# Kernel optimization log

Measured on AMD Instinct MI355X. Metric: run time of the kernel, lower is better.

Reference implementation:

```python
import jax, jax.numpy as jnp
import numpy as np


def setup_inputs() -> dict:
    key = jax.random.key(0)
    k0, k1, k2, k3 = jax.random.split(key, 4)
    N, D, DEG, B = 20000, 128, 32, 1024
    features = jax.random.normal(k0, (N, D), jnp.float32)
    neighbors = jax.random.randint(k1, (N, DEG), 0, N, dtype=jnp.int32)
    train_index = jax.random.randint(k2, (B,), 0, N, dtype=jnp.int32)
    W = jax.random.normal(k3, (1, 2 * D), jnp.float32) * (1.0 / np.sqrt(2 * D))
    b = jnp.zeros((1,), jnp.float32)
    return {"features": features, "W": W, "b": b, "neighbors": neighbors,
            "train_index": train_index, "walk_times": 8, "batch_size": B}


def reference(features, W, b, neighbors, train_index, walk_times, batch_size):
    N, D = features.shape
    B = train_index.shape[0]
    rows = jnp.arange(B)[:, None]                       # [B,1]
    self_oh = jax.nn.one_hot(train_index, N, dtype=jnp.float32)  # [B,N]

    # Dense adjacency rows of the start nodes (== adj_sparse[batch] densified)
    nb0 = neighbors[train_index]                        # [B,deg]
    adj0 = jnp.zeros((B, N), jnp.float32).at[rows, nb0].set(1.0)

    chosen = self_oh                                    # visited mask (start node marked)
    candi_mask = (adj0 - chosen) > 0.0                  # non-self candidates

    # Per-edge learned score: relu(Linear(concat(f_x, f_y))) == relu(fx@Wx + fy@Wy + b)
    Wx, Wy = W[0, :D], W[0, D:]
    sx = features[train_index] @ Wx                     # [B]
    sy = features[nb0] @ Wy                             # [B,deg]
    s = jax.nn.relu(sx[:, None] + sy + b[0])            # [B,deg]
    scored = jnp.zeros((B, N), jnp.float32).at[rows, nb0].set(s)
    candi = jnp.where(candi_mask, scored, 0.0)
    # rows with no (or all-zero-scored) candidates fall back to a self-loop of weight 1
    candi = jnp.where((candi.sum(axis=1) == 0.0)[:, None], self_oh, candi)

    keys = jax.random.split(jax.random.key(42), walk_times)

    def step(carry, k):
        candi, chosen = carry
        # degenerate rows: resample the start node (safe fallback for empty support)
        p = jnp.where((candi.sum(axis=1) == 0.0)[:, None], self_oh, candi)
        # multinomial(p, 1) via Gumbel-max (categorical with probs proportional to p)
        logp = jnp.where(p > 0.0, jnp.log(jnp.where(p > 0.0, p, 1.0)), -jnp.inf)
        g = jax.random.gumbel(k, (p.shape[0], p.shape[1]), jnp.float32)
        new = jnp.argmax(logp + g, axis=1)              # [B]
        chosen = jnp.maximum(chosen, jax.nn.one_hot(new, p.shape[1], dtype=jnp.float32))
        adj_new = jnp.zeros_like(candi).at[rows, neighbors[new]].set(1.0)
        candi = ((candi - chosen + adj_new) > 0.0).astype(jnp.float32)
        return (candi, chosen), new

    (_, _), steps = jax.lax.scan(step, (candi, chosen), keys)  # steps: [T,B]
    walks = jnp.concatenate(
        [train_index[:, None].astype(jnp.int32), steps.T.astype(jnp.int32)], axis=1)
    return walks
```

## Files before the change

kernel.cpp:

```cpp
#include <hip/hip_runtime.h>
#include <cstdint>

namespace {

constexpr int N    = 20000;
constexpr int D    = 128;
constexpr int DEG  = 32;
constexpr int BB   = 1024;
constexpr int T    = 8;
constexpr int NW   = (N + 31) / 32;
constexpr int MAXC = 384;

__device__ __forceinline__ uint32_t rotl32(uint32_t x, int n) {
  return (x << n) | (x >> (32 - n));
}

__device__ __forceinline__ void threefry2x32(uint32_t k0, uint32_t k1,
                                             uint32_t x0, uint32_t x1,
                                             uint32_t& o0, uint32_t& o1) {
  const uint32_t ks2 = k0 ^ k1 ^ 0x1BD11BDAu;
  x0 += k0; x1 += k1;
#define TF_ROUND(r) { x0 += x1; x1 = rotl32(x1, (r)); x1 ^= x0; }
  TF_ROUND(13) TF_ROUND(15) TF_ROUND(26) TF_ROUND(6)
  x0 += k1;  x1 += ks2 + 1u;
  TF_ROUND(17) TF_ROUND(29) TF_ROUND(16) TF_ROUND(24)
  x0 += ks2; x1 += k0 + 2u;
  TF_ROUND(13) TF_ROUND(15) TF_ROUND(26) TF_ROUND(6)
  x0 += k0;  x1 += k1 + 3u;
  TF_ROUND(17) TF_ROUND(29) TF_ROUND(16) TF_ROUND(24)
  x0 += k1;  x1 += ks2 + 4u;
  TF_ROUND(13) TF_ROUND(15) TF_ROUND(26) TF_ROUND(6)
  x0 += ks2; x1 += k0 + 5u;
#undef TF_ROUND
  o0 = x0; o1 = x1;
}

__device__ __forceinline__ uint32_t rbits(uint32_t k0, uint32_t k1, uint32_t j) {
  uint32_t o0, o1;
  threefry2x32(k0, k1, 0u, j, o0, o1);
  return o0 ^ o1;
}

__device__ __forceinline__ float gumbel_f32(uint32_t bits) {
  const uint32_t mant = bits >> 9;
  const float u = (mant == 0u) ? 1.17549435e-38f
                               : (__uint_as_float(0x3F800000u | mant) - 1.0f);
  const float inner = -(float)log((double)u);
  return -(float)log((double)inner);
}

__device__ __forceinline__ uint32_t f2ord(float f) {
  const uint32_t b = __float_as_uint(f);
  return (b & 0x80000000u) ? ~b : (b | 0x80000000u);
}

template <int CTRL>
__device__ __forceinline__ uint32_t dppmov(uint32_t v) {
  return (uint32_t)__builtin_amdgcn_update_dpp((int)v, (int)v, CTRL, 0xF, 0xF, false);
}

__device__ __forceinline__ void wave_max64(uint32_t& hi, uint32_t& lo) {
#define RL(CTRL) { const uint32_t oh = dppmov<CTRL>(hi), ol = dppmov<CTRL>(lo); \
    if (oh > hi || (oh == hi && ol > lo)) { hi = oh; lo = ol; } }
  RL(0x111) RL(0x112) RL(0x114) RL(0x118) RL(0x142) RL(0x143)
#undef RL
  hi = (uint32_t)__builtin_amdgcn_readlane((int)hi, 63);
  lo = (uint32_t)__builtin_amdgcn_readlane((int)lo, 63);
}

__global__ __launch_bounds__(64)
void walk_kernel(const float* __restrict__ features,
                 const float* __restrict__ W,
                 const float* __restrict__ bptr,
                 const int*   __restrict__ neighbors,
                 const int*   __restrict__ train_index,
                 int* __restrict__ out)
{
  __shared__ uint32_t candM[NW];
  __shared__ uint32_t chosenM[NW];
  __shared__ int      lst[2][MAXC];
  __shared__ float    val0[DEG];
  __shared__ int      pendC[16];
  __shared__ float    pendV[16];

  const int lane = threadIdx.x;
  const int r    = blockIdx.x;
  const int self = train_index[r];
  const uint32_t rN = (uint32_t)(r * N);
  const uint64_t lower = (1ULL << lane) - 1ULL;

  int nbj = -1;
  if (lane < DEG) nbj = neighbors[(size_t)self * DEG + lane];

  for (int i = lane; i < NW; i += 64) { candM[i] = 0u; chosenM[i] = 0u; }

  uint32_t sk0, sk1;
  threefry2x32(0u, 42u, 0u, (uint32_t)lane, sk0, sk1);

  const float bval = bptr[0];
  const float* frow = features + (size_t)self * D;
  float acc = frow[lane] * W[lane] + frow[lane + 64] * W[lane + 64];
  for (int m = 1; m < 64; m <<= 1) acc += __shfl_xor(acc, m);
  const float sx = acc;

  float sval = 0.0f;
  if (lane < DEG) {
    const float* g  = features + (size_t)nbj * D;
    const float* wy = W + D;
    float a = 0.0f;
    for (int d = 0; d < D; d += 4) {
      const float4 f = *reinterpret_cast<const float4*>(g + d);
      const float4 w = *reinterpret_cast<const float4*>(wy + d);
      a += f.x * w.x; a += f.y * w.y; a += f.z * w.z; a += f.w * w.w;
    }
    sval = fmaxf((sx + a) + bval, 0.0f);
  }

  bool add0 = false;
  if (lane < DEG && nbj != self && sval > 0.0f) {
    const uint32_t w = (uint32_t)nbj >> 5, bit = 1u << (nbj & 31);
    const uint32_t old = atomicOr(&candM[w], bit);
    add0 = !(old & bit);
  }
  const uint64_t m0 = __ballot(add0);
  if (add0) {
    const int p = (int)__popcll(m0 & lower);
    lst[0][p] = nbj; val0[p] = sval;
  }
  int cnt = (int)__popcll(m0);
  if (lane == 0) {
    chosenM[(uint32_t)self >> 5] |= 1u << (self & 31);
    if (cnt == 0) {
      lst[0][0] = self; val0[0] = 1.0f;
      candM[(uint32_t)self >> 5] |= 1u << (self & 31);
    }
  }
  if (cnt == 0) cnt = 1;

  int cur = 0;
  for (int k = 0; k < T; ++k) {
    const uint32_t kk0 = (uint32_t)__builtin_amdgcn_readlane((int)sk0, k);
    const uint32_t kk1 = (uint32_t)__builtin_amdgcn_readlane((int)sk1, k);

    uint32_t hi = 0u, lo = 0u;
    if (k == 0) {
      for (int i = lane; i < cnt; i += 64) {
        const int c = lst[cur][i];
        const float v = (float)log((double)val0[i])
                      + gumbel_f32(rbits(kk0, kk1, rN + (uint32_t)c));
        const uint32_t h = f2ord(v), l = 0x7FFFFFFFu - (uint32_t)c;
        if (h > hi || (h == hi && l > lo)) { hi = h; lo = l; }
      }
    } else {
      for (int i = lane; i < cnt; i += 128) {
        const int c = lst[cur][i];
        const uint32_t h = rbits(kk0, kk1, rN + (uint32_t)c) >> 9;
        const uint32_t l = 0x7FFFFFFFu - (uint32_t)c;
        uint32_t h2 = 0u, l2 = 0u;
        const int i2 = i + 64;
        if (i2 < cnt) {
          const int c2 = lst[cur][i2];
          h2 = rbits(kk0, kk1, rN + (uint32_t)c2) >> 9;
          l2 = 0x7FFFFFFFu - (uint32_t)c2;
        }
        if (h  > hi || (h  == hi && l  > lo)) { hi = h;  lo = l;  }
        if (h2 > hi || (h2 == hi && l2 > lo)) { hi = h2; lo = l2; }
      }
    }
    wave_max64(hi, lo);
    const int nn = (lo == 0u) ? self : (int)(0x7FFFFFFFu - lo);

    int nb = -1;
    if (lane < DEG) nb = neighbors[(size_t)nn * DEG + lane];

    if (lane == 0) {
      out[r * (T + 1) + k + 1] = nn;
      chosenM[(uint32_t)nn >> 5] |= 1u << (nn & 31);
    }

    int nc = 0, pc = 0;
    for (int i0 = 0; i0 < cnt; i0 += 64) {
      const int i = i0 + lane;
      const bool valid = (i < cnt);
      int c = 0;
      if (valid) c = lst[cur][i];
      bool keep = false, pnd = false;
      if (valid) {
        const uint32_t w = (uint32_t)c >> 5, bit = 1u << (c & 31);
        const bool ch = (c == nn) || ((chosenM[w] & bit) != 0u);
        keep = !ch; pnd = ch;
      }
      const uint64_t mk = __ballot(keep);
      const uint64_t mp = __ballot(pnd);
      if (keep) lst[cur ^ 1][nc + (int)__popcll(mk & lower)] = c;
      if (pnd) {
        const int q = pc + (int)__popcll(mp & lower);
        pendC[q] = c; pendV[q] = (k == 0) ? val0[i] : 1.0f;
      }
      nc += (int)__popcll(mk); pc += (int)__popcll(mp);
    }

    for (int q = 0; q < pc; ++q) {
      const int p = pendC[q];
      const float v = pendV[q];
      const bool isadj = __any(lane < DEG && nb == p);
      if ((v - 1.0f) + (isadj ? 1.0f : 0.0f) > 0.0f) {
        if (lane == 0) lst[cur ^ 1][nc] = p;
        ++nc;
      }
    }

    bool added = false;
    if (lane < DEG && nb != nn) {
      const uint32_t w = (uint32_t)nb >> 5, bit = 1u << (nb & 31);
      if (!(chosenM[w] & bit) && !(candM[w] & bit)) {
        const uint32_t old = atomicOr(&candM[w], bit);
        added = !(old & bit);
      }
    }
    const uint64_t ma = __ballot(added);
    if (added) lst[cur ^ 1][nc + (int)__popcll(ma & lower)] = nb;
    nc += (int)__popcll(ma);

    cnt = nc;
    cur ^= 1;
  }
  if (lane == 0) out[r * (T + 1)] = self;
}

}

extern "C" void kernel_launch(void* const* d_in, const int* in_sizes, int n_in,
                              void* d_out, int out_size, void* d_ws, size_t ws_size,
                              hipStream_t stream) {
  const float* features  = (const float*)d_in[0];
  const float* W         = (const float*)d_in[1];
  const float* b         = (const float*)d_in[2];
  const int*   neighbors = (const int*)d_in[3];
  const int*   tindex    = (const int*)d_in[4];
  int* out = (int*)d_out;

  hipLaunchKernelGGL(walk_kernel, dim3(BB), dim3(64), 0, stream,
                     features, W, b, neighbors, tindex, out);
}
```

Measured before the change: 25.55 us.

## Maintain candidate list in place with swap-remove and tracked zombie entries

Replaces the per-step double-buffered compaction of the candidate list with a single in-place list. Only the chosen node is removed, by swapping in the last element, and up to four 'zombie' chosen-but-still-adjacent entries are tracked in registers and re-tested each step. This removes the full rescan of the candidate list and the pending-list pass every step. In exchange it adds search loops and more control flow, and it caps tracked zombies at four. Because swap-remove reorders the list, the order of candidates differs from before.

```diff
diff --git a/kernel.cpp b/kernel.cpp
--- a/kernel.cpp
+++ b/kernel.cpp
@@ -78,10 +78,8 @@
 {
   __shared__ uint32_t candM[NW];
   __shared__ uint32_t chosenM[NW];
-  __shared__ int      lst[2][MAXC];
+  __shared__ int      lst[MAXC];
   __shared__ float    val0[DEG];
-  __shared__ int      pendC[16];
-  __shared__ float    pendV[16];
 
   const int lane = threadIdx.x;
   const int r    = blockIdx.x;
@@ -125,41 +123,41 @@
   const uint64_t m0 = __ballot(add0);
   if (add0) {
     const int p = (int)__popcll(m0 & lower);
-    lst[0][p] = nbj; val0[p] = sval;
+    lst[p] = nbj; val0[p] = sval;
   }
   int cnt = (int)__popcll(m0);
   if (lane == 0) {
     chosenM[(uint32_t)self >> 5] |= 1u << (self & 31);
     if (cnt == 0) {
-      lst[0][0] = self; val0[0] = 1.0f;
+      lst[0] = self; val0[0] = 1.0f;
       candM[(uint32_t)self >> 5] |= 1u << (self & 31);
     }
   }
   if (cnt == 0) cnt = 1;
 
-  int cur = 0;
+  int zom0 = 0, zom1 = 0, zom2 = 0, zom3 = 0, zmask = 0;
+
   for (int k = 0; k < T; ++k) {
     const uint32_t kk0 = (uint32_t)__builtin_amdgcn_readlane((int)sk0, k);
     const uint32_t kk1 = (uint32_t)__builtin_amdgcn_readlane((int)sk1, k);
 
     uint32_t hi = 0u, lo = 0u;
     if (k == 0) {
-      for (int i = lane; i < cnt; i += 64) {
-        const int c = lst[cur][i];
-        const float v = (float)log((double)val0[i])
+      if (lane < cnt) {
+        const int c = lst[lane];
+        const float v = (float)log((double)val0[lane])
                       + gumbel_f32(rbits(kk0, kk1, rN + (uint32_t)c));
-        const uint32_t h = f2ord(v), l = 0x7FFFFFFFu - (uint32_t)c;
-        if (h > hi || (h == hi && l > lo)) { hi = h; lo = l; }
+        hi = f2ord(v); lo = 0x7FFFFFFFu - (uint32_t)c;
       }
     } else {
       for (int i = lane; i < cnt; i += 128) {
-        const int c = lst[cur][i];
+        const int c = lst[i];
         const uint32_t h = rbits(kk0, kk1, rN + (uint32_t)c) >> 9;
         const uint32_t l = 0x7FFFFFFFu - (uint32_t)c;
         uint32_t h2 = 0u, l2 = 0u;
         const int i2 = i + 64;
         if (i2 < cnt) {
-          const int c2 = lst[cur][i2];
+          const int c2 = lst[i2];
           h2 = rbits(kk0, kk1, rN + (uint32_t)c2) >> 9;
           l2 = 0x7FFFFFFFu - (uint32_t)c2;
         }
@@ -168,7 +166,8 @@
       }
     }
     wave_max64(hi, lo);
-    const int nn = (lo == 0u) ? self : (int)(0x7FFFFFFFu - lo);
+    const bool haveList = (cnt > 0);
+    const int nn = haveList ? (int)(0x7FFFFFFFu - lo) : self;
 
     int nb = -1;
     if (lane < DEG) nb = neighbors[(size_t)nn * DEG + lane];
@@ -178,36 +177,56 @@
       chosenM[(uint32_t)nn >> 5] |= 1u << (nn & 31);
     }
 
-    int nc = 0, pc = 0;
-    for (int i0 = 0; i0 < cnt; i0 += 64) {
-      const int i = i0 + lane;
-      const bool valid = (i < cnt);
-      int c = 0;
-      if (valid) c = lst[cur][i];
-      bool keep = false, pnd = false;
-      if (valid) {
-        const uint32_t w = (uint32_t)c >> 5, bit = 1u << (c & 31);
-        const bool ch = (c == nn) || ((chosenM[w] & bit) != 0u);
-        keep = !ch; pnd = ch;
-      }
-      const uint64_t mk = __ballot(keep);
-      const uint64_t mp = __ballot(pnd);
-      if (keep) lst[cur ^ 1][nc + (int)__popcll(mk & lower)] = c;
-      if (pnd) {
-        const int q = pc + (int)__popcll(mp & lower);
-        pendC[q] = c; pendV[q] = (k == 0) ? val0[i] : 1.0f;
-      }
-      nc += (int)__popcll(mk); pc += (int)__popcll(mp);
-    }
-
-    for (int q = 0; q < pc; ++q) {
-      const int p = pendC[q];
-      const float v = pendV[q];
-      const bool isadj = __any(lane < DEG && nb == p);
-      if ((v - 1.0f) + (isadj ? 1.0f : 0.0f) > 0.0f) {
-        if (lane == 0) lst[cur ^ 1][nc] = p;
-        ++nc;
-      }
+    int pos = -1; float v0f = 1.0f;
+    if (haveList) {
+      for (int i = lane; i < cnt; i += 64) {
+        if (lst[i] == nn) { pos = i; if (k == 0) v0f = val0[i]; }
+      }
+      const uint64_t f = __ballot(pos >= 0);
+      const int src = (int)(__ffsll((unsigned long long)f) - 1);
+      pos = __shfl(pos, src);
+      if (k == 0) v0f = __shfl(v0f, src);
+    }
+
+    const bool adNN = __any(nb == nn);
+    const bool stay = haveList &&
+        ((k == 0) ? (((v0f - 1.0f) + (adNN ? 1.0f : 0.0f)) > 0.0f) : adNN);
+    const bool wasZ = ((zmask & 1) && zom0 == nn) || ((zmask & 2) && zom1 == nn) ||
+                      ((zmask & 4) && zom2 == nn) || ((zmask & 8) && zom3 == nn);
+
+    if (haveList && !stay) {
+      if (pos != cnt - 1) { if (lane == 0) lst[pos] = lst[cnt - 1]; }
+      --cnt;
+      if (wasZ) {
+        if ((zmask & 1) && zom0 == nn) zmask &= ~1;
+        else if ((zmask & 2) && zom1 == nn) zmask &= ~2;
+        else if ((zmask & 4) && zom2 == nn) zmask &= ~4;
+        else if ((zmask & 8) && zom3 == nn) zmask &= ~8;
+      }
+    } else if (haveList && stay && !wasZ) {
+      if      (!(zmask & 1)) { zom0 = nn; zmask |= 1; }
+      else if (!(zmask & 2)) { zom1 = nn; zmask |= 2; }
+      else if (!(zmask & 4)) { zom2 = nn; zmask |= 4; }
+      else                   { zom3 = nn; zmask |= 8; }
+    }
+
+    if (zmask) {
+#define ZTEST(BIT, Z) \
+      if ((zmask & BIT) && Z != nn) { \
+        const bool adz = __any(nb == Z); \
+        if (!adz) { \
+          int pz = -1; \
+          for (int i = lane; i < cnt; i += 64) if (lst[i] == Z) pz = i; \
+          const uint64_t fz = __ballot(pz >= 0); \
+          const int sz = (int)(__ffsll((unsigned long long)fz) - 1); \
+          pz = __shfl(pz, sz); \
+          if (pz != cnt - 1) { if (lane == 0) lst[pz] = lst[cnt - 1]; } \
+          --cnt; \
+          zmask &= ~BIT; \
+        } \
+      }
+      ZTEST(1, zom0) ZTEST(2, zom1) ZTEST(4, zom2) ZTEST(8, zom3)
+#undef ZTEST
     }
 
     bool added = false;
@@ -219,11 +238,8 @@
       }
     }
     const uint64_t ma = __ballot(added);
-    if (added) lst[cur ^ 1][nc + (int)__popcll(ma & lower)] = nb;
-    nc += (int)__popcll(ma);
-
-    cnt = nc;
-    cur ^= 1;
+    if (added) lst[cnt + (int)__popcll(ma & lower)] = nb;
+    cnt += (int)__popcll(ma);
   }
   if (lane == 0) out[r * (T + 1)] = self;
 }
```

Result: faster. 24.93 us (-2.5%).
